# Kernel optimization log

Measured on AMD Instinct MI355X. Metric: run time of the kernel, lower is better.

Reference implementation:

```python
import jax, jax.numpy as jnp
import numpy as np

N_TAXA = 32   # N taxa
K = 256       # particles
T = 16        # live subtrees at this step (t = N - r)
R = 16        # merges already done
S = 1024      # alignment sites
A = 4         # DNA alphabet
D = 64        # embedding dim
C = 16        # site-position feature dim
PRIOR_LEN = 0.1


def _expm4(M):
    """Matrix exponential of [..., A, A] via scaling-and-squaring + Taylor."""
    n_sq = 6
    Ms = M / (2.0 ** n_sq)
    I = jnp.eye(M.shape[-1], dtype=M.dtype)
    P = I + Ms
    Tm = Ms
    for i in range(2, 7):
        Tm = jnp.matmul(Tm, Ms) / i
        P = P + Tm
    for _ in range(n_sq):
        P = jnp.matmul(P, P)
    return P


def _stat_probs(emb_ExD, site_SxC, W_stat, W_site):
    # q_matrix_decoder.stat_probs_VxSxA: per-node, per-site stationary probs
    logits = emb_ExD @ W_stat                     # [E, A]
    logits = logits[:, None, :] + site_SxC @ W_site  # [E, S, A]
    return jax.nn.softmax(logits, axis=-1)


def setup_inputs() -> dict:
    key = jax.random.key(0)
    ks = jax.random.split(key, 10)
    ldf = np.zeros(2 * N_TAXA, np.float32)
    for n in range(2, 2 * N_TAXA):
        ldf[n] = ldf[n - 2] + np.log(n)
    return {
        "log_weight_K": jax.random.normal(ks[0], (K,), jnp.float32),
        "branch1_lengths_Kxr": jax.random.uniform(ks[1], (K, R), jnp.float32) * 0.2 + 1e-3,
        "branch2_lengths_Kxr": jax.random.uniform(ks[2], (K, R), jnp.float32) * 0.2 + 1e-3,
        "leaf_counts_Kxt": jnp.ones((K, T), jnp.int32),
        "embeddings_KxtxD": jax.random.normal(ks[3], (K, T, D), jnp.float32),
        "log_felsensteins_KxtxSxA": jax.nn.log_softmax(
            jax.random.normal(ks[4], (K, T, S, A), jnp.float32), axis=-1),
        "log_pi_K": jax.random.normal(ks[5], (K,), jnp.float32),
        "site_positions_SxC": jax.random.uniform(ks[6], (S, C), jnp.float32),
        "W_stat": jax.random.normal(ks[7], (D, A), jnp.float32) * 0.1,
        "W_site": jax.random.normal(ks[8], (C, A), jnp.float32) * 0.1,
        "log_double_factorials_2N": jnp.asarray(ldf),
    }


def reference(log_weight_K, branch1_lengths_Kxr, branch2_lengths_Kxr,
              leaf_counts_Kxt, embeddings_KxtxD, log_felsensteins_KxtxSxA,
              log_pi_K, site_positions_SxC, W_stat, W_site,
              log_double_factorials_2N):
    K_, T_, S_, A_ = log_felsensteins_KxtxSxA.shape
    key = jax.random.key(42)
    kres, ki, koff, ku1, ku2 = jax.random.split(key, 5)

    # ---- SMC categorical resampling over particles ----
    idxK = jax.random.categorical(kres, log_weight_K, shape=(K_,))
    b1r = branch1_lengths_Kxr[idxK]
    b2r = branch2_lengths_Kxr[idxK]
    lc = leaf_counts_Kxt[idxK]
    emb = embeddings_KxtxD[idxK]
    logf = log_felsensteins_KxtxSxA[idxK]
    prev_log_pi = log_pi_K[idxK]

    # ---- proposal (J=1): uniform pair + exponential branch lengths ----
    i = jax.random.randint(ki, (K_,), 0, T_)
    off = jax.random.randint(koff, (K_,), 1, T_)
    j = (i + off) % T_
    idx1 = jnp.minimum(i, j)
    idx2 = jnp.maximum(i, j)
    branch1 = -PRIOR_LEN * jnp.log(jax.random.uniform(ku1, (K_,), minval=1e-6, maxval=1.0))
    branch2 = -PRIOR_LEN * jnp.log(jax.random.uniform(ku2, (K_,), minval=1e-6, maxval=1.0))
    ar = jnp.arange(K_)
    new_emb = 0.5 * (emb[ar, idx1] + emb[ar, idx2])  # [K, D]
    log_v_plus = jnp.log(T_ * (T_ - 1) / 2.0)        # log #pairs

    # ---- merge: put merged value at idx1, move last slot into idx2, drop last ----
    def merge(arr, new_val):
        arr = arr.at[ar, idx1].set(new_val)
        arr = arr.at[ar, idx2].set(arr[ar, T_ - 1])
        return arr[:, :T_ - 1]

    lc_new = merge(lc, lc[ar, idx1] + lc[ar, idx2])   # [K, t-1]
    emb_new = merge(emb, new_emb)                     # [K, t-1, D]

    # ---- Felsenstein pruning step for the merged node ----
    stat = _stat_probs(new_emb, site_positions_SxC, W_stat, W_site)  # [K,S,A]
    Q = jnp.broadcast_to(stat[:, :, None, :], (K_, S_, A_, A_)) - jnp.eye(A_, dtype=stat.dtype)
    P1 = _expm4(Q * branch1[:, None, None, None])  # [K,S,A,A]
    P2 = _expm4(Q * branch2[:, None, None, None])
    f1 = jnp.exp(logf[ar, idx1])  # [K,S,A]
    f2 = jnp.exp(logf[ar, idx2])
    new_logf = (jnp.log(jnp.einsum('ksab,ksb->ksa', P1, f1) + 1e-30)
                + jnp.log(jnp.einsum('ksab,ksb->ksa', P2, f2) + 1e-30))
    logf_new = merge(logf, new_logf)  # [K, t-1, S, A]

    # ---- log pi over the forest: per-subtree likelihood + priors ----
    t_new = T_ - 1
    stat_all = _stat_probs(emb_new.reshape(K_ * t_new, -1), site_positions_SxC,
                           W_stat, W_site).reshape(K_, t_new, S_, A_)
    log_stat = jnp.log(stat_all)
    L = jnp.sum(jax.scipy.special.logsumexp(logf_new + log_stat, axis=-1), axis=-1)  # [K,t-1]
    topo_idx = jnp.clip(2 * lc_new - 3, 0, 2 * N_TAXA - 1)
    topo = -log_double_factorials_2N[topo_idx] * (lc_new >= 2).astype(L.dtype)
    b1_all = jnp.concatenate([b1r, branch1[:, None]], axis=1)  # [K, r+1]
    b2_all = jnp.concatenate([b2r, branch2[:, None]], axis=1)
    prior = (jnp.sum(-b1_all / PRIOR_LEN, axis=1) + jnp.sum(-b2_all / PRIOR_LEN, axis=1)
             - 2.0 * (b1_all.shape[1]) * jnp.log(jnp.asarray(PRIOR_LEN, L.dtype)))
    log_pi_new = jnp.sum(L + topo, axis=1) + prior

    # ---- importance weight ----
    log_v_minus = jnp.log(jnp.maximum(jnp.sum((lc_new > 1).astype(L.dtype), axis=1), 1.0))
    log_weight_new = log_pi_new - prev_log_pi + log_v_minus - log_v_plus
    return log_weight_new
```

## Files before the change

### kernel.cpp

```cpp
#include <hip/hip_runtime.h>
#include <stdint.h>


#define TF_ROT(x0,x1,r) { x0 += x1; x1 = ((x1<<(r))|(x1>>(32-(r)))); x1 ^= x0; }

__host__ __device__ inline void tf2x32(uint32_t k0, uint32_t k1,
                                       uint32_t x0, uint32_t x1,
                                       uint32_t& o0, uint32_t& o1) {
  uint32_t ks2 = k0 ^ k1 ^ 0x1BD11BDAu;
  x0 += k0; x1 += k1;
  TF_ROT(x0,x1,13) TF_ROT(x0,x1,15) TF_ROT(x0,x1,26) TF_ROT(x0,x1,6)
  x0 += k1; x1 += ks2 + 1u;
  TF_ROT(x0,x1,17) TF_ROT(x0,x1,29) TF_ROT(x0,x1,16) TF_ROT(x0,x1,24)
  x0 += ks2; x1 += k0 + 2u;
  TF_ROT(x0,x1,13) TF_ROT(x0,x1,15) TF_ROT(x0,x1,26) TF_ROT(x0,x1,6)
  x0 += k0; x1 += k1 + 3u;
  TF_ROT(x0,x1,17) TF_ROT(x0,x1,29) TF_ROT(x0,x1,16) TF_ROT(x0,x1,24)
  x0 += k1; x1 += ks2 + 4u;
  TF_ROT(x0,x1,13) TF_ROT(x0,x1,15) TF_ROT(x0,x1,26) TF_ROT(x0,x1,6)
  x0 += ks2; x1 += k0 + 5u;
  o0 = x0; o1 = x1;
}

struct Keys {
  uint32_t kres0, kres1;
  uint32_t k2i0, k2i1;
  uint32_t k1o0, k1o1;
  uint32_t k2o0, k2o1;
  uint32_t ku10, ku11;
  uint32_t ku20, ku21;
};

__device__ inline uint32_t rb_fold(uint32_t k0, uint32_t k1, uint32_t i) {
  uint32_t o0, o1;
  tf2x32(k0, k1, 0u, i, o0, o1);
  return o0 ^ o1;
}

__device__ inline float u01f(uint32_t b) {
  return __uint_as_float((b >> 9) | 0x3F800000u) - 1.0f;
}

#define TINYF 1.17549435e-38f

__global__ __launch_bounds__(256) void k_pre(const float* __restrict__ site,
                                             const float* __restrict__ Wsite,
                                             float* __restrict__ eslw,
                                             int* __restrict__ used) {
  int tid = threadIdx.x;
  int s = blockIdx.x * 256 + tid;
  if (blockIdx.x == 0) used[tid] = 0;
  float a0 = 0.f, a1 = 0.f, a2 = 0.f, a3 = 0.f;
#pragma unroll
  for (int c = 0; c < 16; c++) {
    float sc = site[s * 16 + c];
    a0 += sc * Wsite[c * 4 + 0];
    a1 += sc * Wsite[c * 4 + 1];
    a2 += sc * Wsite[c * 4 + 2];
    a3 += sc * Wsite[c * 4 + 3];
  }
  float4 v; v.x = __expf(a0); v.y = __expf(a1); v.z = __expf(a2); v.w = __expf(a3);
  ((float4*)eslw)[s] = v;
}

__global__ __launch_bounds__(256) void k_setup(
    const float* __restrict__ logw, const float* __restrict__ b1r,
    const float* __restrict__ b2r, const int* __restrict__ lc,
    const float* __restrict__ emb, const float* __restrict__ logpi,
    const float* __restrict__ Wstat, const float* __restrict__ ldf,
    float* __restrict__ enlm, float* __restrict__ w1w, float* __restrict__ w2w,
    float* __restrict__ cw, int* __restrict__ pw, int* __restrict__ i1w,
    int* __restrict__ i2w, int* __restrict__ used, Keys kk) {
  int k = blockIdx.x, tid = threadIdx.x;
  __shared__ float sval[256];
  __shared__ int   sidx[256];
  __shared__ int   sh_i1, sh_i2;

  {
    uint32_t b = rb_fold(kk.kres0, kk.kres1, (uint32_t)(k * 256 + tid));
    float u = fmaxf(TINYF, u01f(b) + TINYF);
    float g = -logf(-logf(u));
    sval[tid] = g + logw[tid];
    sidx[tid] = tid;
  }
  __syncthreads();
  for (int st = 128; st > 0; st >>= 1) {
    if (tid < st) {
      float va = sval[tid], vb = sval[tid + st];
      int ia = sidx[tid], ib = sidx[tid + st];
      if (vb > va || (vb == va && ib < ia)) { sval[tid] = vb; sidx[tid] = ib; }
    }
    __syncthreads();
  }
  int p = sidx[0];

  if (tid == 0) {
    used[p] = 1;
    uint32_t i = rb_fold(kk.k2i0, kk.k2i1, (uint32_t)k) & 15u;
    uint32_t h = rb_fold(kk.k1o0, kk.k1o1, (uint32_t)k) % 15u;
    uint32_t l = rb_fold(kk.k2o0, kk.k2o1, (uint32_t)k) % 15u;
    uint32_t off = 1u + (h + l) % 15u;
    uint32_t j = (i + off) & 15u;
    int i1 = (int)(i < j ? i : j);
    int i2 = (int)(i < j ? j : i);
    sh_i1 = i1; sh_i2 = i2;

    const float SUBR = 1.0f - 1e-6f;
    float u1 = fmaxf(1e-6f, u01f(rb_fold(kk.ku10, kk.ku11, (uint32_t)k)) * SUBR + 1e-6f);
    float u2 = fmaxf(1e-6f, u01f(rb_fold(kk.ku20, kk.ku21, (uint32_t)k)) * SUBR + 1e-6f);
    float b1 = -0.1f * logf(u1);
    float b2 = -0.1f * logf(u2);
    w1w[k] = 1.0f - expf(-b1);
    w2w[k] = 1.0f - expf(-b2);
    i1w[k] = i1; i2w[k] = i2; pw[k] = p;

    float sb = b1 + b2;
    for (int r = 0; r < 16; r++) sb += b1r[p * 16 + r] + b2r[p * 16 + r];
    float prior = -sb / 0.1f - 34.0f * logf(0.1f);

    float topo_sum = 0.0f; int cnt = 0;
    for (int t = 0; t < 15; t++) {
      int lct;
      if (t == i1)      lct = lc[p * 16 + i1] + lc[p * 16 + i2];
      else if (t == i2) lct = lc[p * 16 + 15];
      else              lct = lc[p * 16 + t];
      int ti = 2 * lct - 3; ti = ti < 0 ? 0 : (ti > 63 ? 63 : ti);
      if (lct >= 2) topo_sum -= ldf[ti];
      if (lct > 1) cnt++;
    }
    float log_v_minus = logf(fmaxf((float)cnt, 1.0f));
    float log_v_plus = logf(120.0f);
    cw[k] = prior + topo_sum - logpi[p] + log_v_minus - log_v_plus;
  }
  __syncthreads();

  if (tid < 4) {
    int a = tid, i1 = sh_i1, i2 = sh_i2, p2 = sidx[0];
    const float* e1 = emb + ((size_t)p2 * 16 + i1) * 64;
    const float* e2 = emb + ((size_t)p2 * 16 + i2) * 64;
    float acc = 0.0f;
    for (int d = 0; d < 64; d++) acc += 0.5f * (e1[d] + e2[d]) * Wstat[d * 4 + a];
    enlm[k * 4 + a] = __expf(acc);
  }
}

__global__ __launch_bounds__(256) void k_lorig(
    const float* __restrict__ lfg, const float* __restrict__ eslw,
    const float* __restrict__ emb, const float* __restrict__ Wstat,
    const int* __restrict__ used, float* __restrict__ Lpart) {
  int p = blockIdx.y, sblk = blockIdx.x, tid = threadIdx.x;
  if (used[p] == 0) return;
  __shared__ float enl[64];
  __shared__ float sred[16 * 4];
  if (tid < 64) {
    int t = tid >> 2, a = tid & 3;
    const float4* e4 = (const float4*)(emb + ((size_t)p * 16 + t) * 64);
    float acc = 0.0f;
#pragma unroll
    for (int d4 = 0; d4 < 16; d4++) {
      float4 e = e4[d4];
      acc += e.x * Wstat[(d4 * 4 + 0) * 4 + a] + e.y * Wstat[(d4 * 4 + 1) * 4 + a] +
             e.z * Wstat[(d4 * 4 + 2) * 4 + a] + e.w * Wstat[(d4 * 4 + 3) * 4 + a];
    }
    enl[tid] = __expf(acc);
  }
  __syncthreads();
  int s = sblk * 256 + tid;
  const float4 esl = ((const float4*)eslw)[s];
  const float* base = lfg + (size_t)p * 65536;

  float acc[16];
#pragma unroll
  for (int t = 0; t < 16; t++) {
    float4 lf = *(const float4*)(base + t * 4096 + s * 4);
    float w0 = enl[t * 4 + 0] * esl.x, w1 = enl[t * 4 + 1] * esl.y;
    float w2 = enl[t * 4 + 2] * esl.z, w3 = enl[t * 4 + 3] * esl.w;
    float S1 = w0 + w1 + w2 + w3;
    float S2 = __expf(lf.x) * w0 + __expf(lf.y) * w1 +
               __expf(lf.z) * w2 + __expf(lf.w) * w3;
    acc[t] = __log2f(S2) - __log2f(S1);
  }
#pragma unroll
  for (int t = 0; t < 16; t++) {
    float v = acc[t];
    for (int o = 32; o > 0; o >>= 1) v += __shfl_down(v, o, 64);
    if ((tid & 63) == 0) sred[t * 4 + (tid >> 6)] = v;
  }
  __syncthreads();
  if (tid < 16) {
    float s4 = sred[tid * 4 + 0] + sred[tid * 4 + 1] + sred[tid * 4 + 2] + sred[tid * 4 + 3];
    Lpart[((size_t)p * 4 + sblk) * 16 + tid] = s4 * 0.69314718056f;
  }
}

__global__ __launch_bounds__(1024) void k_fin(
    const float* __restrict__ lfg, const float* __restrict__ eslw,
    const float* __restrict__ enlm, const float* __restrict__ w1w,
    const float* __restrict__ w2w, const int* __restrict__ pw,
    const int* __restrict__ i1w, const int* __restrict__ i2w,
    const float* __restrict__ cw, const float* __restrict__ Lpart,
    float* __restrict__ out) {
  int k = blockIdx.x, tid = threadIdx.x;
  __shared__ float sred[16];
  int p = pw[k], i1 = i1w[k], i2 = i2w[k];
  float w1 = w1w[k], w2 = w2w[k];
  float om1 = 1.0f - w1, om2 = 1.0f - w2;
  float m0 = enlm[k * 4 + 0], m1 = enlm[k * 4 + 1];
  float m2 = enlm[k * 4 + 2], m3 = enlm[k * 4 + 3];
  const float* base = lfg + (size_t)p * 65536;

  int s = tid;
  const float4 esl = ((const float4*)eslw)[s];
  float t0 = m0 * esl.x, t1 = m1 * esl.y, t2 = m2 * esl.z, t3 = m3 * esl.w;
  float T = t0 + t1 + t2 + t3;
  float invT = 1.0f / T;
  float4 lf1 = *(const float4*)(base + i1 * 4096 + s * 4);
  float4 lf2 = *(const float4*)(base + i2 * 4096 + s * 4);
  float f10 = __expf(lf1.x), f11 = __expf(lf1.y), f12 = __expf(lf1.z), f13 = __expf(lf1.w);
  float f20 = __expf(lf2.x), f21 = __expf(lf2.y), f22 = __expf(lf2.z), f23 = __expf(lf2.w);
  float dot1 = (t0 * f10 + t1 * f11 + t2 * f12 + t3 * f13) * invT;
  float dot2 = (t0 * f20 + t1 * f21 + t2 * f22 + t3 * f23) * invT;
  float n0 = __logf(om1 * f10 + w1 * dot1 + 1e-30f) + __logf(om2 * f20 + w2 * dot2 + 1e-30f);
  float n1 = __logf(om1 * f11 + w1 * dot1 + 1e-30f) + __logf(om2 * f21 + w2 * dot2 + 1e-30f);
  float n2 = __logf(om1 * f12 + w1 * dot1 + 1e-30f) + __logf(om2 * f22 + w2 * dot2 + 1e-30f);
  float n3 = __logf(om1 * f13 + w1 * dot1 + 1e-30f) + __logf(om2 * f23 + w2 * dot2 + 1e-30f);
  float S2 = __expf(n0) * t0 + __expf(n1) * t1 + __expf(n2) * t2 + __expf(n3) * t3;
  float tot = __logf(S2) - __logf(T);

  for (int o = 32; o > 0; o >>= 1) tot += __shfl_down(tot, o, 64);
  if ((tid & 63) == 0) sred[tid >> 6] = tot;
  __syncthreads();
  if (tid < 64) {
    int t = tid & 15;
    float coef = (t == i1 || t == i2) ? 0.0f : 1.0f;
    float v = coef * Lpart[(size_t)p * 64 + tid];
    if (tid < 16) v += sred[tid];
    for (int o = 32; o > 0; o >>= 1) v += __shfl_down(v, o, 64);
    if (tid == 0) out[k] = cw[k] + v;
  }
}

extern "C" void kernel_launch(void* const* d_in, const int* in_sizes, int n_in,
                              void* d_out, int out_size, void* d_ws, size_t ws_size,
                              hipStream_t stream) {
  const float* logw  = (const float*)d_in[0];
  const float* b1r   = (const float*)d_in[1];
  const float* b2r   = (const float*)d_in[2];
  const int*   lc    = (const int*)d_in[3];
  const float* emb   = (const float*)d_in[4];
  const float* lfg   = (const float*)d_in[5];
  const float* logpi = (const float*)d_in[6];
  const float* site  = (const float*)d_in[7];
  const float* Wstat = (const float*)d_in[8];
  const float* Wsite = (const float*)d_in[9];
  const float* ldf   = (const float*)d_in[10];

  char* w = (char*)d_ws;
  float* eslw  = (float*)w; w += 1024 * 4 * 4;
  float* enlm  = (float*)w; w += 256 * 4 * 4;
  float* w1w   = (float*)w; w += 256 * 4;
  float* w2w   = (float*)w; w += 256 * 4;
  float* cw    = (float*)w; w += 256 * 4;
  int*   pw    = (int*)w;   w += 256 * 4;
  int*   i1w   = (int*)w;   w += 256 * 4;
  int*   i2w   = (int*)w;   w += 256 * 4;
  int*   used  = (int*)w;   w += 256 * 4;
  float* Lpart = (float*)w; w += 256 * 64 * 4;

  uint32_t S0[5], S1[5];
  for (uint32_t i = 0; i < 5; i++) tf2x32(0u, 42u, 0u, i, S0[i], S1[i]);
  Keys kk;
  kk.kres0 = S0[0]; kk.kres1 = S1[0];
  kk.ku10  = S0[3]; kk.ku11  = S1[3];
  kk.ku20  = S0[4]; kk.ku21  = S1[4];
  {
    uint32_t a0, a1, b0, b1;
    tf2x32(S0[1], S1[1], 0u, 0u, a0, a1);
    tf2x32(S0[1], S1[1], 0u, 1u, b0, b1);
    (void)a0; (void)a1;
    kk.k2i0 = b0; kk.k2i1 = b1;
  }
  {
    uint32_t a0, a1, b0, b1;
    tf2x32(S0[2], S1[2], 0u, 0u, a0, a1);
    tf2x32(S0[2], S1[2], 0u, 1u, b0, b1);
    kk.k1o0 = a0; kk.k1o1 = a1;
    kk.k2o0 = b0; kk.k2o1 = b1;
  }

  k_pre<<<4, 256, 0, stream>>>(site, Wsite, eslw, used);
  k_setup<<<256, 256, 0, stream>>>(logw, b1r, b2r, lc, emb, logpi, Wstat, ldf,
                                   enlm, w1w, w2w, cw, pw, i1w, i2w, used, kk);
  dim3 gC(4, 256);
  k_lorig<<<gC, 256, 0, stream>>>(lfg, eslw, emb, Wstat, used, Lpart);
  k_fin<<<256, 1024, 0, stream>>>(lfg, eslw, enlm, w1w, w2w, pw, i1w, i2w,
                                  cw, Lpart, (float*)d_out);
}
```

Measured before the change: 129.3 us.

## Fuse site precompute into setup and merge-likelihood into per-parent kernel

```diff
diff --git a/kernel.cpp b/kernel.cpp
--- a/kernel.cpp
+++ b/kernel.cpp
@@ -43,42 +43,40 @@
 
 #define TINYF 1.17549435e-38f
 
-__global__ __launch_bounds__(256) void k_pre(const float* __restrict__ site,
-                                             const float* __restrict__ Wsite,
-                                             float* __restrict__ eslw,
-                                             int* __restrict__ used) {
-  int tid = threadIdx.x;
-  int s = blockIdx.x * 256 + tid;
-  if (blockIdx.x == 0) used[tid] = 0;
-  float a0 = 0.f, a1 = 0.f, a2 = 0.f, a3 = 0.f;
-#pragma unroll
-  for (int c = 0; c < 16; c++) {
-    float sc = site[s * 16 + c];
-    a0 += sc * Wsite[c * 4 + 0];
-    a1 += sc * Wsite[c * 4 + 1];
-    a2 += sc * Wsite[c * 4 + 2];
-    a3 += sc * Wsite[c * 4 + 3];
-  }
-  float4 v; v.x = __expf(a0); v.y = __expf(a1); v.z = __expf(a2); v.w = __expf(a3);
-  ((float4*)eslw)[s] = v;
-}
-
-__global__ __launch_bounds__(256) void k_setup(
+__global__ __launch_bounds__(256) void k_sf(
     const float* __restrict__ logw, const float* __restrict__ b1r,
     const float* __restrict__ b2r, const int* __restrict__ lc,
     const float* __restrict__ emb, const float* __restrict__ logpi,
     const float* __restrict__ Wstat, const float* __restrict__ ldf,
-    float* __restrict__ enlm, float* __restrict__ w1w, float* __restrict__ w2w,
+    const float* __restrict__ site, const float* __restrict__ Wsite,
+    float* __restrict__ eslw, float* __restrict__ enlm,
+    float* __restrict__ w1w, float* __restrict__ w2w,
     float* __restrict__ cw, int* __restrict__ pw, int* __restrict__ i1w,
-    int* __restrict__ i2w, int* __restrict__ used, Keys kk) {
-  int k = blockIdx.x, tid = threadIdx.x;
+    int* __restrict__ i2w, Keys kk) {
+  int b = blockIdx.x, tid = threadIdx.x;
+  if (b >= 256) {
+    int s = (b - 256) * 256 + tid;
+    float a0 = 0.f, a1 = 0.f, a2 = 0.f, a3 = 0.f;
+#pragma unroll
+    for (int c = 0; c < 16; c++) {
+      float sc = site[s * 16 + c];
+      a0 += sc * Wsite[c * 4 + 0];
+      a1 += sc * Wsite[c * 4 + 1];
+      a2 += sc * Wsite[c * 4 + 2];
+      a3 += sc * Wsite[c * 4 + 3];
+    }
+    float4 v; v.x = __expf(a0); v.y = __expf(a1); v.z = __expf(a2); v.w = __expf(a3);
+    ((float4*)eslw)[s] = v;
+    return;
+  }
+  int k = b;
   __shared__ float sval[256];
   __shared__ int   sidx[256];
   __shared__ int   sh_i1, sh_i2;
 
   {
-    uint32_t b = rb_fold(kk.kres0, kk.kres1, (uint32_t)(k * 256 + tid));
-    float u = fmaxf(TINYF, u01f(b) + TINYF);
+    uint32_t bb = rb_fold(kk.kres0, kk.kres1, (uint32_t)(k * 256 + tid));
+    float u = fmaxf(TINYF, u01f(bb) + TINYF);
     float g = -logf(-logf(u));
     sval[tid] = g + logw[tid];
     sidx[tid] = tid;
@@ -95,7 +93,6 @@
   int p = sidx[0];
 
   if (tid == 0) {
-    used[p] = 1;
     uint32_t i = rb_fold(kk.k2i0, kk.k2i1, (uint32_t)k) & 15u;
     uint32_t h = rb_fold(kk.k1o0, kk.k1o1, (uint32_t)k) % 15u;
     uint32_t l = rb_fold(kk.k2o0, kk.k2o1, (uint32_t)k) % 15u;
@@ -147,11 +144,22 @@
 __global__ __launch_bounds__(256) void k_lorig(
     const float* __restrict__ lfg, const float* __restrict__ eslw,
     const float* __restrict__ emb, const float* __restrict__ Wstat,
-    const int* __restrict__ used, float* __restrict__ Lpart) {
+    const int* __restrict__ pw, const int* __restrict__ i1w,
+    const int* __restrict__ i2w, const float* __restrict__ w1w,
+    const float* __restrict__ w2w, const float* __restrict__ enlm,
+    float* __restrict__ Lpart, float* __restrict__ Lm) {
   int p = blockIdx.y, sblk = blockIdx.x, tid = threadIdx.x;
-  if (used[p] == 0) return;
+  __shared__ int klist[256];
+  __shared__ int kcount;
   __shared__ float enl[64];
   __shared__ float sred[16 * 4];
+  __shared__ float sredm[4];
+  if (tid == 0) kcount = 0;
+  __syncthreads();
+  if (pw[tid] == p) { int sl = atomicAdd(&kcount, 1); klist[sl] = tid; }
+  __syncthreads();
+  if (kcount == 0) return;
+
   if (tid < 64) {
     int t = tid >> 2, a = tid & 3;
     const float4* e4 = (const float4*)(emb + ((size_t)p * 16 + t) * 64);
@@ -191,53 +199,55 @@
     float s4 = sred[tid * 4 + 0] + sred[tid * 4 + 1] + sred[tid * 4 + 2] + sred[tid * 4 + 3];
     Lpart[((size_t)p * 4 + sblk) * 16 + tid] = s4 * 0.69314718056f;
   }
-}
-
-__global__ __launch_bounds__(1024) void k_fin(
-    const float* __restrict__ lfg, const float* __restrict__ eslw,
-    const float* __restrict__ enlm, const float* __restrict__ w1w,
-    const float* __restrict__ w2w, const int* __restrict__ pw,
+
+  for (int q = 0; q < kcount; q++) {
+    int kq = klist[q];
+    int i1 = i1w[kq], i2 = i2w[kq];
+    float w1 = w1w[kq], w2 = w2w[kq];
+    float om1 = 1.0f - w1, om2 = 1.0f - w2;
+    float m0 = enlm[kq * 4 + 0], m1 = enlm[kq * 4 + 1];
+    float m2 = enlm[kq * 4 + 2], m3 = enlm[kq * 4 + 3];
+    float t0 = m0 * esl.x, t1 = m1 * esl.y, t2 = m2 * esl.z, t3 = m3 * esl.w;
+    float T = t0 + t1 + t2 + t3;
+    float invT = 1.0f / T;
+    float4 lf1 = *(const float4*)(base + i1 * 4096 + s * 4);
+    float4 lf2 = *(const float4*)(base + i2 * 4096 + s * 4);
+    float f10 = __expf(lf1.x), f11 = __expf(lf1.y), f12 = __expf(lf1.z), f13 = __expf(lf1.w);
+    float f20 = __expf(lf2.x), f21 = __expf(lf2.y), f22 = __expf(lf2.z), f23 = __expf(lf2.w);
+    float dot1 = (t0 * f10 + t1 * f11 + t2 * f12 + t3 * f13) * invT;
+    float dot2 = (t0 * f20 + t1 * f21 + t2 * f22 + t3 * f23) * invT;
+    float n0 = __logf(om1 * f10 + w1 * dot1 + 1e-30f) + __logf(om2 * f20 + w2 * dot2 + 1e-30f);
+    float n1 = __logf(om1 * f11 + w1 * dot1 + 1e-30f) + __logf(om2 * f21 + w2 * dot2 + 1e-30f);
+    float n2 = __logf(om1 * f12 + w1 * dot1 + 1e-30f) + __logf(om2 * f22 + w2 * dot2 + 1e-30f);
+    float n3 = __logf(om1 * f13 + w1 * dot1 + 1e-30f) + __logf(om2 * f23 + w2 * dot2 + 1e-30f);
+    float S2 = __expf(n0) * t0 + __expf(n1) * t1 + __expf(n2) * t2 + __expf(n3) * t3;
+    float tot = __logf(S2) - __logf(T);
+    for (int o = 32; o > 0; o >>= 1) tot += __shfl_down(tot, o, 64);
+    if ((tid & 63) == 0) sredm[tid >> 6] = tot;
+    __syncthreads();
+    if (tid == 0)
+      Lm[kq * 4 + sblk] = sredm[0] + sredm[1] + sredm[2] + sredm[3];
+    __syncthreads();
+  }
+}
+
+__global__ __launch_bounds__(256) void k_out(
+    const float* __restrict__ cw, const float* __restrict__ Lpart,
+    const float* __restrict__ Lm, const int* __restrict__ pw,
     const int* __restrict__ i1w, const int* __restrict__ i2w,
-    const float* __restrict__ cw, const float* __restrict__ Lpart,
     float* __restrict__ out) {
-  int k = blockIdx.x, tid = threadIdx.x;
-  __shared__ float sred[16];
+  int k = threadIdx.x;
   int p = pw[k], i1 = i1w[k], i2 = i2w[k];
-  float w1 = w1w[k], w2 = w2w[k];
-  float om1 = 1.0f - w1, om2 = 1.0f - w2;
-  float m0 = enlm[k * 4 + 0], m1 = enlm[k * 4 + 1];
-  float m2 = enlm[k * 4 + 2], m3 = enlm[k * 4 + 3];
-  const float* base = lfg + (size_t)p * 65536;
-
-  int s = tid;
-  const float4 esl = ((const float4*)eslw)[s];
-  float t0 = m0 * esl.x, t1 = m1 * esl.y, t2 = m2 * esl.z, t3 = m3 * esl.w;
-  float T = t0 + t1 + t2 + t3;
-  float invT = 1.0f / T;
-  float4 lf1 = *(const float4*)(base + i1 * 4096 + s * 4);
-  float4 lf2 = *(const float4*)(base + i2 * 4096 + s * 4);
-  float f10 = __expf(lf1.x), f11 = __expf(lf1.y), f12 = __expf(lf1.z), f13 = __expf(lf1.w);
-  float f20 = __expf(lf2.x), f21 = __expf(lf2.y), f22 = __expf(lf2.z), f23 = __expf(lf2.w);
-  float dot1 = (t0 * f10 + t1 * f11 + t2 * f12 + t3 * f13) * invT;
-  float dot2 = (t0 * f20 + t1 * f21 + t2 * f22 + t3 * f23) * invT;
-  float n0 = __logf(om1 * f10 + w1 * dot1 + 1e-30f) + __logf(om2 * f20 + w2 * dot2 + 1e-30f);
-  float n1 = __logf(om1 * f11 + w1 * dot1 + 1e-30f) + __logf(om2 * f21 + w2 * dot2 + 1e-30f);
-  float n2 = __logf(om1 * f12 + w1 * dot1 + 1e-30f) + __logf(om2 * f22 + w2 * dot2 + 1e-30f);
-  float n3 = __logf(om1 * f13 + w1 * dot1 + 1e-30f) + __logf(om2 * f23 + w2 * dot2 + 1e-30f);
-  float S2 = __expf(n0) * t0 + __expf(n1) * t1 + __expf(n2) * t2 + __expf(n3) * t3;
-  float tot = __logf(S2) - __logf(T);
-
-  for (int o = 32; o > 0; o >>= 1) tot += __shfl_down(tot, o, 64);
-  if ((tid & 63) == 0) sred[tid >> 6] = tot;
-  __syncthreads();
-  if (tid < 64) {
-    int t = tid & 15;
-    float coef = (t == i1 || t == i2) ? 0.0f : 1.0f;
-    float v = coef * Lpart[(size_t)p * 64 + tid];
-    if (tid < 16) v += sred[tid];
-    for (int o = 32; o > 0; o >>= 1) v += __shfl_down(v, o, 64);
-    if (tid == 0) out[k] = cw[k] + v;
-  }
+  const float* Lp = Lpart + (size_t)p * 64;
+  float sum = cw[k];
+#pragma unroll
+  for (int sb = 0; sb < 4; sb++) {
+    float ss = Lm[k * 4 + sb];
+    for (int t = 0; t < 16; t++)
+      if (t != i1 && t != i2) ss += Lp[sb * 16 + t];
+    sum += ss;
+  }
+  out[k] = sum;
 }
 
 extern "C" void kernel_launch(void* const* d_in, const int* in_sizes, int n_in,
@@ -264,8 +274,8 @@
   int*   pw    = (int*)w;   w += 256 * 4;
   int*   i1w   = (int*)w;   w += 256 * 4;
   int*   i2w   = (int*)w;   w += 256 * 4;
-  int*   used  = (int*)w;   w += 256 * 4;
   float* Lpart = (float*)w; w += 256 * 64 * 4;
+  float* Lm    = (float*)w; w += 256 * 4 * 4;
 
   uint32_t S0[5], S1[5];
   for (uint32_t i = 0; i < 5; i++) tf2x32(0u, 42u, 0u, i, S0[i], S1[i]);
@@ -288,11 +298,11 @@
     kk.k2o0 = b0; kk.k2o1 = b1;
   }
 
-  k_pre<<<4, 256, 0, stream>>>(site, Wsite, eslw, used);
-  k_setup<<<256, 256, 0, stream>>>(logw, b1r, b2r, lc, emb, logpi, Wstat, ldf,
-                                   enlm, w1w, w2w, cw, pw, i1w, i2w, used, kk);
+  k_sf<<<260, 256, 0, stream>>>(logw, b1r, b2r, lc, emb, logpi, Wstat, ldf,
+                                site, Wsite, eslw, enlm, w1w, w2w, cw,
+                                pw, i1w, i2w, kk);
   dim3 gC(4, 256);
-  k_lorig<<<gC, 256, 0, stream>>>(lfg, eslw, emb, Wstat, used, Lpart);
-  k_fin<<<256, 1024, 0, stream>>>(lfg, eslw, enlm, w1w, w2w, pw, i1w, i2w,
-                                  cw, Lpart, (float*)d_out);
-}
+  k_lorig<<<gC, 256, 0, stream>>>(lfg, eslw, emb, Wstat, pw, i1w, i2w,
+                                  w1w, w2w, enlm, Lpart, Lm);
+  k_out<<<1, 256, 0, stream>>>(cw, Lpart, Lm, pw, i1w, i2w, (float*)d_out);
+}
```

Measured after the change: 141.9 us. +9.7%, slower.
